# Optimization experiments

Measured on AMD Instinct MI355X. Metric: run time of the kernel, lower is better.

## Reference

```python
import jax, jax.numpy as jnp
import numpy as np
import math

NUM_EXPERTS = 8
CAP_FACTOR = 1.25
MIN_CAPACITY = 4

def _capacity(num_tokens, num_experts):
    cap = math.floor(CAP_FACTOR * num_tokens / num_experts)
    cap += cap % 2
    return max(cap, MIN_CAPACITY)

def setup_inputs() -> dict:
    key = jax.random.key(0)
    k1, k2, k3, k4 = jax.random.split(key, 4)
    tokens, d_model, d_ff, E = 8192, 1024, 4096, NUM_EXPERTS
    x = jax.random.normal(k1, (tokens, d_model), dtype=jnp.float32)
    gate_weight = jax.random.normal(k2, (E, d_model), dtype=jnp.float32) * math.sqrt(0.1 / d_model)
    expert_weight = jax.random.normal(k3, (E, d_model, d_ff), dtype=jnp.float32) * 0.02
    expert_bias = jax.random.normal(k4, (E, 1, d_ff), dtype=jnp.float32) * 0.02
    return {"x": x, "gate_weight": gate_weight, "expert_weight": expert_weight, "expert_bias": expert_bias}

def reference(x, gate_weight, expert_weight, expert_bias):
    tokens, d_model = x.shape
    E = gate_weight.shape[0]
    capacity = _capacity(tokens, E)
    # FP32 gate (Switch-style)
    gate_logits = jnp.dot(x.astype(jnp.float32), gate_weight.astype(jnp.float32).T)  # [s, E]
    logits = jax.nn.softmax(gate_logits, axis=-1)  # auto_cast_softmax in fp32
    # Top-1 routing, select_policy='first'
    top1_idx = jnp.argmax(gate_logits, axis=-1)  # argmax over raw gate output
    mask = jax.nn.one_hot(top1_idx, E, dtype=jnp.int32)  # [s, E]
    # aux load-balancing loss (training path)
    me = jnp.mean(logits, axis=0)
    ce = jnp.mean(mask.astype(jnp.float32), axis=0)
    l_aux = E * jnp.sum(me * ce)
    # cumsum-based capacity ranking
    ranks = jnp.cumsum(mask, axis=0) - 1  # [s, E]
    mask = mask * (ranks < capacity).astype(jnp.int32)
    ranks_tok = jnp.sum(mask * ranks, axis=-1)  # [s]
    rank_oh = jax.nn.one_hot(ranks_tok, capacity, dtype=logits.dtype)  # [s, c]
    weight = mask.astype(logits.dtype) * logits  # [s, E]
    combine_weights = weight[:, :, None] * rank_oh[:, None, :]  # [s, E, c]
    sec_mask = combine_weights != 0  # bool dispatch mask
    # scatter dispatch: [s,E,c] x [s,d] -> [E,c,d]
    dispatched = jnp.einsum("sec,sd->ecd", sec_mask.astype(x.dtype), x)
    # per-expert front linear: [E,c,d] x [E,d,f] -> [E,c,f]
    out = jnp.einsum("ecd,edf->ecf", dispatched, expert_weight) + expert_bias
    return out, combine_weights, l_aux
```

## Files before the change

### kernel.cpp

```cpp
#include <hip/hip_runtime.h>
#include <hip/hip_bf16.h>

#define TOKENS 8192
#define DM 1024
#define DFF 4096
#define NE 8
#define CAP 1280
#define ECAP (NE*CAP)
#define OUT_ELEMS ((size_t)NE*CAP*DFF)
#define CMB_ELEMS ((size_t)TOKENS*NE*CAP)
#define ZROW TOKENS
#define GBK 32

typedef __attribute__((ext_vector_type(8))) short short8;
typedef __attribute__((ext_vector_type(16))) float f32x16;
typedef __attribute__((ext_vector_type(4))) float f4;

__device__ inline ushort f2bf(float f) {
    __hip_bfloat16 h = __float2bfloat16(f);
    return *reinterpret_cast<ushort*>(&h);
}

__device__ __forceinline__ void gload16(const ushort* g, short* l) {
    __builtin_amdgcn_global_load_lds(
        (const __attribute__((address_space(1))) void*)g,
        (__attribute__((address_space(3))) void*)l, 16, 0, 0);
}

__global__ __launch_bounds__(256) void gate_kernel(const float* __restrict__ x,
        const float* __restrict__ gw, float* __restrict__ probs8, int* __restrict__ top1,
        ushort* __restrict__ xbf) {
    int wave = threadIdx.x >> 6;
    int lane = threadIdx.x & 63;
    int t = blockIdx.x * 4 + wave;
    const float* xrow = x + (size_t)t * DM;
    float4 xv[4];
    #pragma unroll
    for (int j = 0; j < 4; ++j) xv[j] = *(const float4*)(xrow + lane * 4 + j * 256);
    ushort* xbrow = xbf + (size_t)t * DM;
    #pragma unroll
    for (int j = 0; j < 4; ++j) {
        ushort4 o;
        o.x = f2bf(xv[j].x); o.y = f2bf(xv[j].y); o.z = f2bf(xv[j].z); o.w = f2bf(xv[j].w);
        *(ushort4*)(xbrow + lane * 4 + j * 256) = o;
    }
    float logit[8];
    #pragma unroll
    for (int e = 0; e < 8; ++e) {
        const float* g = gw + e * DM;
        float s = 0.f;
        #pragma unroll
        for (int j = 0; j < 4; ++j) {
            float4 gv = *(const float4*)(g + lane * 4 + j * 256);
            s += xv[j].x * gv.x + xv[j].y * gv.y + xv[j].z * gv.z + xv[j].w * gv.w;
        }
        #pragma unroll
        for (int off = 32; off >= 1; off >>= 1) s += __shfl_xor(s, off);
        logit[e] = s;
    }
    if (lane == 0) {
        int bi = 0; float bv = logit[0];
        #pragma unroll
        for (int e = 1; e < 8; ++e) if (logit[e] > bv) { bv = logit[e]; bi = e; }
        float se = 0.f, p[8];
        #pragma unroll
        for (int e = 0; e < 8; ++e) { p[e] = expf(logit[e] - bv); se += p[e]; }
        float inv = 1.f / se;
        #pragma unroll
        for (int e = 0; e < 8; ++e) probs8[t * 8 + e] = p[e] * inv;
        top1[t] = bi;
    }
    if (blockIdx.x == 0) {
        ushort4 z; z.x = z.y = z.z = z.w = 0;
        *(ushort4*)(xbf + (size_t)ZROW * DM + threadIdx.x * 4) = z;
    }
}

__global__ __launch_bounds__(512) void cvtw_rank_kernel(
        const float* __restrict__ w, ushort* __restrict__ wt,
        const int* __restrict__ top1, const float* __restrict__ probs8,
        int* __restrict__ slot_token, int* __restrict__ pos,
        int* __restrict__ cnts, float* __restrict__ laux_out) {
    __shared__ __align__(16) char smem[TOKENS * 4 + 64 * 4 + 8 * 4];
    const int tid = threadIdx.x;
    if (blockIdx.x == 0) {
        int* t1s = (int*)smem;
        float* red = (float*)(smem + TOKENS * 4);
        int* cnt_sh = (int*)(smem + TOKENS * 4 + 64 * 4);
        int w8 = tid >> 6;
        int lane = tid & 63;
        for (int i = tid; i < TOKENS; i += 512) t1s[i] = top1[i];
        for (int i = tid; i < ECAP; i += 512) slot_token[i] = ZROW;
        for (int i = tid; i < TOKENS; i += 512) pos[i] = -1;

        float ps[8];
        #pragma unroll
        for (int e = 0; e < 8; ++e) ps[e] = 0.f;
        for (int t = tid; t < TOKENS; t += 512) {
            float4 a = *(const float4*)(probs8 + t * 8);
            float4 b = *(const float4*)(probs8 + t * 8 + 4);
            ps[0] += a.x; ps[1] += a.y; ps[2] += a.z; ps[3] += a.w;
            ps[4] += b.x; ps[5] += b.y; ps[6] += b.z; ps[7] += b.w;
        }
        #pragma unroll
        for (int e = 0; e < 8; ++e) {
            #pragma unroll
            for (int off = 32; off >= 1; off >>= 1) ps[e] += __shfl_xor(ps[e], off);
        }
        if (lane == 0) {
            #pragma unroll
            for (int e = 0; e < 8; ++e) red[w8 * 8 + e] = ps[e];
        }
        __syncthreads();

        int base = 0;
        for (int t0 = 0; t0 < TOKENS; t0 += 256) {
            #pragma unroll
            for (int q = 0; q < 4; ++q) {
                int t = t0 + q * 64 + lane;
                bool mine = (t1s[t] == w8);
                unsigned long long m = __ballot(mine);
                if (mine) {
                    int r = base + __popcll(m & ((1ull << lane) - 1ull));
                    if (r < CAP) { slot_token[w8 * CAP + r] = t; pos[t] = w8 * CAP + r; }
                }
                base += __popcll(m);
            }
        }
        if (lane == 0) { cnt_sh[w8] = base; cnts[w8] = (base < CAP) ? base : CAP; }
        __syncthreads();
        if (tid == 0) {
            float la = 0.f;
            #pragma unroll
            for (int e = 0; e < 8; ++e) {
                float me = 0.f;
                #pragma unroll
                for (int wv = 0; wv < 8; ++wv) me += red[wv * 8 + e];
                la += (me / (float)TOKENS) * ((float)cnt_sh[e] / (float)TOKENS);
            }
            laux_out[0] = la * (float)NE;
        }
        return;
    }
    float (*tile)[65] = (float(*)[65])smem;
    int b = blockIdx.x - 1;
    int e = b >> 11;
    int rem = b & 2047;
    int n0 = (rem & 63) * 64;
    int k0 = (rem >> 6) * 32;
    const float* we = w + (size_t)e * DM * DFF;
    int c = tid & 63, r0 = tid >> 6;
    #pragma unroll
    for (int i = 0; i < 4; ++i) {
        int r = r0 + i * 8;
        tile[r][c] = we[(size_t)(k0 + r) * DFF + n0 + c];
    }
    __syncthreads();
    ushort* wte = wt + (size_t)e * DFF * DM;
    int kc = tid & 31, nr0 = tid >> 5;
    #pragma unroll
    for (int i = 0; i < 4; ++i) {
        int nr = nr0 + i * 16;
        wte[(size_t)(n0 + nr) * DM + k0 + kc] = f2bf(tile[kc][nr]);
    }
}

__global__ __launch_bounds__(512, 2) void gemm_kernel(
    const ushort* __restrict__ xbf,
    const ushort* __restrict__ wt,
    const float*  __restrict__ bias,
    const int*    __restrict__ slot_token,
    const int*    __restrict__ cnts,
    float* __restrict__ out,
    const int*    __restrict__ pos,
    const float*  __restrict__ probs8,
    float* __restrict__ cmb,
    int do_combine)
{
    const int bid = blockIdx.x;
    const int e   = bid & 7;
    const int rem = bid >> 3;
    const int nt  = rem & 15;
    const int mt  = rem >> 4;
    __shared__ __align__(16) short lds[4][16384];
    const int tid  = threadIdx.x;
    const int lane = tid & 63;
    const int wave = tid >> 6;
    const int wr = wave >> 2;
    const int wc = wave & 3;
    const int ln31 = lane & 31, lh = lane >> 5;
    const int tbeg = bid * 16;
    const bool has_cmb = do_combine && (bid < 512);

    float* orow = out + ((size_t)(e * CAP + mt * 256)) * DFF + (size_t)nt * 256;

    if (mt * 256 >= cnts[e]) {
        int c4 = tid & 63;
        int r0b = tid >> 6;
        f4 bv4 = *(const f4*)(bias + e * DFF + nt * 256 + c4 * 4);
        for (int r = r0b; r < 256; r += 8)
            __builtin_nontemporal_store(bv4, (f4*)(orow + (size_t)r * DFF + c4 * 4));
        if (has_cmb) {
            for (int i = 0; i < 16; ++i) {
                int tok = tbeg + i;
                int p = pos[tok];
                int ee = (p < 0) ? 0 : (p / CAP);
                float val = probs8[tok * 8 + ee];
                f4* row = (f4*)(cmb + (size_t)tok * ECAP);
                #pragma unroll
                for (int k = 0; k < 5; ++k) {
                    int b4 = (tid + k * 512) * 4;
                    f4 v;
                    v.x = (b4 + 0 == p) ? val : 0.f;
                    v.y = (b4 + 1 == p) ? val : 0.f;
                    v.z = (b4 + 2 == p) ? val : 0.f;
                    v.w = (b4 + 3 == p) ? val : 0.f;
                    __builtin_nontemporal_store(v, row + tid + k * 512);
                }
            }
        }
        return;
    }

    const int r0 = tid >> 2;
    const int kg = (tid & 3) ^ ((tid >> 3) & 3);
    const int tokA0 = slot_token[e * CAP + mt * 256 + r0];
    const int tokA1 = slot_token[e * CAP + mt * 256 + 128 + r0];
    const ushort* aptr0 = xbf + (size_t)tokA0 * DM + kg * 8;
    const ushort* aptr1 = xbf + (size_t)tokA1 * DM + kg * 8;
    const ushort* bptr0 = wt + ((size_t)e * DFF + (size_t)nt * 256 + r0) * DM + kg * 8;
    const ushort* bptr1 = bptr0 + (size_t)128 * DM;

    #define STAGE(T) do { \
        short* base_ = &lds[(T) & 3][0]; \
        size_t ko_ = (size_t)(T) * GBK; \
        gload16(aptr0 + ko_, base_ + tid * 8); \
        gload16(aptr1 + ko_, base_ + 4096 + tid * 8); \
        gload16(bptr0 + ko_, base_ + 8192 + tid * 8); \
        gload16(bptr1 + ko_, base_ + 12288 + tid * 8); \
    } while (0)

    int aoff[8], boff[4];
    #pragma unroll
    for (int s = 0; s < 2; ++s) {
        #pragma unroll
        for (int mi = 0; mi < 4; ++mi) {
            int r = wr * 128 + mi * 32 + ln31;
            int c = lh + 2 * s;
            aoff[s * 4 + mi] = (r * 4 + (c ^ ((r >> 1) & 3))) * 8;
        }
        #pragma unroll
        for (int ni = 0; ni < 2; ++ni) {
            int rn = wc * 64 + ni * 32 + ln31;
            int c = lh + 2 * s;
            boff[s * 2 + ni] = 8192 + (rn * 4 + (c ^ ((rn >> 1) & 3))) * 8;
        }
    }

    f4* cmb_p = (f4*)cmb + (size_t)tbeg * (ECAP / 4);
    int kpart = 0, ntok = 0;
    int cur_p = -1, nxt_p = -1;
    float cur_val = 0.f, nxt_val = 0.f;
    if (has_cmb) {
        cur_p = pos[tbeg];
        { int ee = (cur_p < 0) ? 0 : (cur_p / CAP); cur_val = probs8[tbeg * 8 + ee]; }
        nxt_p = pos[tbeg + 1];
        { int ee = (nxt_p < 0) ? 0 : (nxt_p / CAP); nxt_val = probs8[(tbeg + 1) * 8 + ee]; }
    }
    #define CSTORE() do { if (has_cmb) { \
        int b4_ = (tid + kpart * 512) * 4; \
        f4 v_; \
        v_.x = (b4_ + 0 == cur_p) ? cur_val : 0.f; \
        v_.y = (b4_ + 1 == cur_p) ? cur_val : 0.f; \
        v_.z = (b4_ + 2 == cur_p) ? cur_val : 0.f; \
        v_.w = (b4_ + 3 == cur_p) ? cur_val : 0.f; \
        __builtin_nontemporal_store(v_, cmb_p + tid + kpart * 512); \
        if (++kpart == 5) { \
            kpart = 0; cmb_p += ECAP / 4; ++ntok; \
            cur_p = nxt_p; cur_val = nxt_val; \
            if (ntok + 1 < 16) { \
                nxt_p = pos[tbeg + ntok + 1]; \
                int ee_ = (nxt_p < 0) ? 0 : (nxt_p / CAP); \
                nxt_val = probs8[(tbeg + ntok + 1) * 8 + ee_]; \
            } \
        } \
    } } while (0)

    f32x16 acc[4][2];
    #pragma unroll
    for (int mi = 0; mi < 4; ++mi)
        #pragma unroll
        for (int ni = 0; ni < 2; ++ni)
            acc[mi][ni] = (f32x16)(0.f);

    STAGE(0); STAGE(1); STAGE(2);
    for (int t = 0; t < 32; ++t) {
        if (t < 29) {
            STAGE(t + 3);
            asm volatile("s_waitcnt vmcnt(12)" ::: "memory");
        } else if (t == 29) {
            asm volatile("s_waitcnt vmcnt(8)" ::: "memory");
        } else if (t == 30) {
            asm volatile("s_waitcnt vmcnt(4)" ::: "memory");
        } else {
            asm volatile("s_waitcnt vmcnt(0)" ::: "memory");
        }
        __builtin_amdgcn_s_barrier();
        __builtin_amdgcn_sched_barrier(0);

        const short* L = &lds[t & 3][0];
        __builtin_amdgcn_s_setprio(1);
        #pragma unroll
        for (int s = 0; s < 2; ++s) {
            short8 af[4], bfr[2];
            #pragma unroll
            for (int ni = 0; ni < 2; ++ni) bfr[ni] = *(const short8*)(L + boff[s * 2 + ni]);
            #pragma unroll
            for (int mi = 0; mi < 4; ++mi) af[mi] = *(const short8*)(L + aoff[s * 4 + mi]);
            #pragma unroll
            for (int mi = 0; mi < 4; ++mi)
                #pragma unroll
                for (int ni = 0; ni < 2; ++ni)
                    acc[mi][ni] = __builtin_amdgcn_mfma_f32_32x32x16_bf16(af[mi], bfr[ni], acc[mi][ni], 0, 0, 0);
        }
        __builtin_amdgcn_s_setprio(0);
        CSTORE(); CSTORE();
        if (t < 16) CSTORE();
        __builtin_amdgcn_sched_barrier(0);
        asm volatile("" ::: "memory");
        __builtin_amdgcn_s_barrier();
        asm volatile("" ::: "memory");
    }
    #undef STAGE
    #undef CSTORE

    #pragma unroll
    for (int ni = 0; ni < 2; ++ni) {
        int c = wc * 64 + ni * 32 + ln31;
        float bv = bias[e * DFF + nt * 256 + c];
        #pragma unroll
        for (int mi = 0; mi < 4; ++mi) {
            #pragma unroll
            for (int reg = 0; reg < 16; ++reg) {
                int r = wr * 128 + mi * 32 + (reg & 3) + 8 * (reg >> 2) + 4 * lh;
                __builtin_nontemporal_store(acc[mi][ni][reg] + bv,
                    orow + (size_t)r * DFF + c);
            }
        }
    }
}

__global__ __launch_bounds__(256) void combine_kernel(const int* __restrict__ pos,
        const float* __restrict__ probs8, float* __restrict__ cmb) {
    int tok = blockIdx.x;
    int p = pos[tok];
    int e = p / CAP;
    float val = probs8[tok * 8 + (e < 0 ? 0 : e)];
    f4* row = (f4*)(cmb + (size_t)tok * ECAP);
    #pragma unroll
    for (int k = 0; k < 10; ++k) {
        int c = threadIdx.x + k * 256;
        int b4 = c * 4;
        f4 v;
        v.x = (b4 + 0 == p) ? val : 0.f;
        v.y = (b4 + 1 == p) ? val : 0.f;
        v.z = (b4 + 2 == p) ? val : 0.f;
        v.w = (b4 + 3 == p) ? val : 0.f;
        __builtin_nontemporal_store(v, row + c);
    }
}

extern "C" void kernel_launch(void* const* d_in, const int* in_sizes, int n_in,
                              void* d_out, int out_size, void* d_ws, size_t ws_size,
                              hipStream_t stream) {
    const float* x  = (const float*)d_in[0];
    const float* gw = (const float*)d_in[1];
    const float* ew = (const float*)d_in[2];
    const float* eb = (const float*)d_in[3];

    float* out = (float*)d_out;
    float* cmb = out + OUT_ELEMS;
    float* laux_out = cmb + CMB_ELEMS;

    float* probs8 = (float*)d_ws;
    int* top1 = (int*)(probs8 + TOKENS * 8);
    int* slot_token = top1 + TOKENS;
    int* pos = slot_token + ECAP;
    int* cnts = pos + TOKENS;

    const size_t SMALL = 1 << 20;
    const size_t WT_ELEMS_ = (size_t)NE * DFF * DM;
    const size_t XBF_ELEMS_ = (size_t)(TOKENS + 1) * DM;
    bool big_ws = ws_size >= SMALL + (WT_ELEMS_ + XBF_ELEMS_) * sizeof(ushort);
    ushort* wtbf = big_ws ? (ushort*)((char*)d_ws + SMALL) : (ushort*)cmb;
    ushort* xbf  = wtbf + WT_ELEMS_;

    gate_kernel<<<TOKENS / 4, 256, 0, stream>>>(x, gw, probs8, top1, xbf);
    cvtw_rank_kernel<<<16385, 512, 0, stream>>>(ew, wtbf, top1, probs8,
                                                slot_token, pos, cnts, laux_out);
    if (big_ws) {
        gemm_kernel<<<640, 512, 0, stream>>>(xbf, wtbf, eb, slot_token, cnts, out,
                                             pos, probs8, cmb, 1);
    } else {
        gemm_kernel<<<640, 512, 0, stream>>>(xbf, wtbf, eb, slot_token, cnts, out,
                                             pos, probs8, cmb, 0);
        combine_kernel<<<TOKENS, 256, 0, stream>>>(pos, probs8, cmb);
    }
}
```

Measured before the change: 193.2 us.

## Shrink GEMM tiles to 128x128 with 256 threads and double buffering

The expert GEMM tile drops from 256x256 with 512 threads and a 4-stage LDS pipeline to 128x128 with 256 threads and a 2-stage pipeline, spread over 2560 blocks. Each block writes its combine-weight rows after the GEMM instead of interleaving the stores inside the k-loop. The aim is more blocks per CU and better load balance across the ragged per-expert token counts. In exchange, each tile reuses its operands less, issues more global loads per flop, and has a shallower prefetch depth to hide latency.

```diff
diff --git a/kernel.cpp b/kernel.cpp
--- a/kernel.cpp
+++ b/kernel.cpp
@@ -165,7 +165,7 @@
     }
 }
 
-__global__ __launch_bounds__(512, 2) void gemm_kernel(
+__global__ __launch_bounds__(256, 3) void gemm_kernel(
     const ushort* __restrict__ xbf,
     const ushort* __restrict__ wt,
     const float*  __restrict__ bias,
@@ -180,171 +180,135 @@
     const int bid = blockIdx.x;
     const int e   = bid & 7;
     const int rem = bid >> 3;
-    const int nt  = rem & 15;
-    const int mt  = rem >> 4;
-    __shared__ __align__(16) short lds[4][16384];
+    const int nt  = rem & 31;
+    const int mt  = rem >> 5;
+    __shared__ __align__(16) short lds[2][8192];
     const int tid  = threadIdx.x;
     const int lane = tid & 63;
     const int wave = tid >> 6;
-    const int wr = wave >> 2;
-    const int wc = wave & 3;
+    const int wr = wave >> 1;
+    const int wc = wave & 1;
     const int ln31 = lane & 31, lh = lane >> 5;
-    const int tbeg = bid * 16;
-    const bool has_cmb = do_combine && (bid < 512);
-
-    float* orow = out + ((size_t)(e * CAP + mt * 256)) * DFF + (size_t)nt * 256;
-
-    if (mt * 256 >= cnts[e]) {
-        int c4 = tid & 63;
-        int r0b = tid >> 6;
-        f4 bv4 = *(const f4*)(bias + e * DFF + nt * 256 + c4 * 4);
-        for (int r = r0b; r < 256; r += 8)
+    const int tbeg = bid * 4;
+    const bool has_cmb = do_combine && (bid < 2048);
+
+    float* orow = out + ((size_t)(e * CAP + mt * 128)) * DFF + (size_t)nt * 128;
+
+    if (mt * 128 >= cnts[e]) {
+        int c4 = tid & 31;
+        int r0b = tid >> 5;
+        f4 bv4 = *(const f4*)(bias + e * DFF + nt * 128 + c4 * 4);
+        for (int r = r0b; r < 128; r += 8)
             __builtin_nontemporal_store(bv4, (f4*)(orow + (size_t)r * DFF + c4 * 4));
-        if (has_cmb) {
-            for (int i = 0; i < 16; ++i) {
-                int tok = tbeg + i;
-                int p = pos[tok];
-                int ee = (p < 0) ? 0 : (p / CAP);
-                float val = probs8[tok * 8 + ee];
-                f4* row = (f4*)(cmb + (size_t)tok * ECAP);
-                #pragma unroll
-                for (int k = 0; k < 5; ++k) {
-                    int b4 = (tid + k * 512) * 4;
-                    f4 v;
-                    v.x = (b4 + 0 == p) ? val : 0.f;
-                    v.y = (b4 + 1 == p) ? val : 0.f;
-                    v.z = (b4 + 2 == p) ? val : 0.f;
-                    v.w = (b4 + 3 == p) ? val : 0.f;
-                    __builtin_nontemporal_store(v, row + tid + k * 512);
+    } else {
+        const int r0 = tid >> 2;
+        const int kg = (tid & 3) ^ ((tid >> 3) & 3);
+        const int tokA0 = slot_token[e * CAP + mt * 128 + r0];
+        const int tokA1 = slot_token[e * CAP + mt * 128 + 64 + r0];
+        const ushort* aptr0 = xbf + (size_t)tokA0 * DM + kg * 8;
+        const ushort* aptr1 = xbf + (size_t)tokA1 * DM + kg * 8;
+        const ushort* bptr0 = wt + ((size_t)e * DFF + (size_t)nt * 128 + r0) * DM + kg * 8;
+        const ushort* bptr1 = bptr0 + (size_t)64 * DM;
+
+        #define STAGE(T) do { \
+            short* base_ = &lds[(T) & 1][0]; \
+            size_t ko_ = (size_t)(T) * GBK; \
+            gload16(aptr0 + ko_, base_ + tid * 8); \
+            gload16(aptr1 + ko_, base_ + 2048 + tid * 8); \
+            gload16(bptr0 + ko_, base_ + 4096 + tid * 8); \
+            gload16(bptr1 + ko_, base_ + 6144 + tid * 8); \
+        } while (0)
+
+        int aoff[4], boff[4];
+        #pragma unroll
+        for (int s = 0; s < 2; ++s) {
+            #pragma unroll
+            for (int mi = 0; mi < 2; ++mi) {
+                int r = wr * 64 + mi * 32 + ln31;
+                int c = lh + 2 * s;
+                aoff[s * 2 + mi] = (r * 4 + (c ^ ((r >> 1) & 3))) * 8;
+            }
+            #pragma unroll
+            for (int ni = 0; ni < 2; ++ni) {
+                int rn = wc * 64 + ni * 32 + ln31;
+                int c = lh + 2 * s;
+                boff[s * 2 + ni] = 4096 + (rn * 4 + (c ^ ((rn >> 1) & 3))) * 8;
+            }
+        }
+
+        f32x16 acc[2][2];
+        #pragma unroll
+        for (int mi = 0; mi < 2; ++mi)
+            #pragma unroll
+            for (int ni = 0; ni < 2; ++ni)
+                acc[mi][ni] = (f32x16)(0.f);
+
+        STAGE(0);
+        for (int t = 0; t < 32; ++t) {
+            if (t < 31) {
+                STAGE(t + 1);
+                asm volatile("s_waitcnt vmcnt(4)" ::: "memory");
+            } else {
+                asm volatile("s_waitcnt vmcnt(0)" ::: "memory");
+            }
+            __builtin_amdgcn_s_barrier();
+            __builtin_amdgcn_sched_barrier(0);
+
+            const short* L = &lds[t & 1][0];
+            __builtin_amdgcn_s_setprio(1);
+            #pragma unroll
+            for (int s = 0; s < 2; ++s) {
+                short8 af[2], bfr[2];
+                #pragma unroll
+                for (int ni = 0; ni < 2; ++ni) bfr[ni] = *(const short8*)(L + boff[s * 2 + ni]);
+                #pragma unroll
+                for (int mi = 0; mi < 2; ++mi) af[mi] = *(const short8*)(L + aoff[s * 2 + mi]);
+                #pragma unroll
+                for (int mi = 0; mi < 2; ++mi)
+                    #pragma unroll
+                    for (int ni = 0; ni < 2; ++ni)
+                        acc[mi][ni] = __builtin_amdgcn_mfma_f32_32x32x16_bf16(af[mi], bfr[ni], acc[mi][ni], 0, 0, 0);
+            }
+            __builtin_amdgcn_s_setprio(0);
+            __builtin_amdgcn_sched_barrier(0);
+            asm volatile("" ::: "memory");
+            __builtin_amdgcn_s_barrier();
+            asm volatile("" ::: "memory");
+        }
+        #undef STAGE
+
+        #pragma unroll
+        for (int ni = 0; ni < 2; ++ni) {
+            int c = wc * 64 + ni * 32 + ln31;
+            float bv = bias[e * DFF + nt * 128 + c];
+            #pragma unroll
+            for (int mi = 0; mi < 2; ++mi) {
+                #pragma unroll
+                for (int reg = 0; reg < 16; ++reg) {
+                    int r = wr * 64 + mi * 32 + (reg & 3) + 8 * (reg >> 2) + 4 * lh;
+                    __builtin_nontemporal_store(acc[mi][ni][reg] + bv,
+                        orow + (size_t)r * DFF + c);
                 }
             }
         }
-        return;
-    }
-
-    const int r0 = tid >> 2;
-    const int kg = (tid & 3) ^ ((tid >> 3) & 3);
-    const int tokA0 = slot_token[e * CAP + mt * 256 + r0];
-    const int tokA1 = slot_token[e * CAP + mt * 256 + 128 + r0];
-    const ushort* aptr0 = xbf + (size_t)tokA0 * DM + kg * 8;
-    const ushort* aptr1 = xbf + (size_t)tokA1 * DM + kg * 8;
-    const ushort* bptr0 = wt + ((size_t)e * DFF + (size_t)nt * 256 + r0) * DM + kg * 8;
-    const ushort* bptr1 = bptr0 + (size_t)128 * DM;
-
-    #define STAGE(T) do { \
-        short* base_ = &lds[(T) & 3][0]; \
-        size_t ko_ = (size_t)(T) * GBK; \
-        gload16(aptr0 + ko_, base_ + tid * 8); \
-        gload16(aptr1 + ko_, base_ + 4096 + tid * 8); \
-        gload16(bptr0 + ko_, base_ + 8192 + tid * 8); \
-        gload16(bptr1 + ko_, base_ + 12288 + tid * 8); \
-    } while (0)
-
-    int aoff[8], boff[4];
-    #pragma unroll
-    for (int s = 0; s < 2; ++s) {
-        #pragma unroll
-        for (int mi = 0; mi < 4; ++mi) {
-            int r = wr * 128 + mi * 32 + ln31;
-            int c = lh + 2 * s;
-            aoff[s * 4 + mi] = (r * 4 + (c ^ ((r >> 1) & 3))) * 8;
-        }
-        #pragma unroll
-        for (int ni = 0; ni < 2; ++ni) {
-            int rn = wc * 64 + ni * 32 + ln31;
-            int c = lh + 2 * s;
-            boff[s * 2 + ni] = 8192 + (rn * 4 + (c ^ ((rn >> 1) & 3))) * 8;
-        }
-    }
-
-    f4* cmb_p = (f4*)cmb + (size_t)tbeg * (ECAP / 4);
-    int kpart = 0, ntok = 0;
-    int cur_p = -1, nxt_p = -1;
-    float cur_val = 0.f, nxt_val = 0.f;
+    }
+
     if (has_cmb) {
-        cur_p = pos[tbeg];
-        { int ee = (cur_p < 0) ? 0 : (cur_p / CAP); cur_val = probs8[tbeg * 8 + ee]; }
-        nxt_p = pos[tbeg + 1];
-        { int ee = (nxt_p < 0) ? 0 : (nxt_p / CAP); nxt_val = probs8[(tbeg + 1) * 8 + ee]; }
-    }
-    #define CSTORE() do { if (has_cmb) { \
-        int b4_ = (tid + kpart * 512) * 4; \
-        f4 v_; \
-        v_.x = (b4_ + 0 == cur_p) ? cur_val : 0.f; \
-        v_.y = (b4_ + 1 == cur_p) ? cur_val : 0.f; \
-        v_.z = (b4_ + 2 == cur_p) ? cur_val : 0.f; \
-        v_.w = (b4_ + 3 == cur_p) ? cur_val : 0.f; \
-        __builtin_nontemporal_store(v_, cmb_p + tid + kpart * 512); \
-        if (++kpart == 5) { \
-            kpart = 0; cmb_p += ECAP / 4; ++ntok; \
-            cur_p = nxt_p; cur_val = nxt_val; \
-            if (ntok + 1 < 16) { \
-                nxt_p = pos[tbeg + ntok + 1]; \
-                int ee_ = (nxt_p < 0) ? 0 : (nxt_p / CAP); \
-                nxt_val = probs8[(tbeg + ntok + 1) * 8 + ee_]; \
-            } \
-        } \
-    } } while (0)
-
-    f32x16 acc[4][2];
-    #pragma unroll
-    for (int mi = 0; mi < 4; ++mi)
-        #pragma unroll
-        for (int ni = 0; ni < 2; ++ni)
-            acc[mi][ni] = (f32x16)(0.f);
-
-    STAGE(0); STAGE(1); STAGE(2);
-    for (int t = 0; t < 32; ++t) {
-        if (t < 29) {
-            STAGE(t + 3);
-            asm volatile("s_waitcnt vmcnt(12)" ::: "memory");
-        } else if (t == 29) {
-            asm volatile("s_waitcnt vmcnt(8)" ::: "memory");
-        } else if (t == 30) {
-            asm volatile("s_waitcnt vmcnt(4)" ::: "memory");
-        } else {
-            asm volatile("s_waitcnt vmcnt(0)" ::: "memory");
-        }
-        __builtin_amdgcn_s_barrier();
-        __builtin_amdgcn_sched_barrier(0);
-
-        const short* L = &lds[t & 3][0];
-        __builtin_amdgcn_s_setprio(1);
-        #pragma unroll
-        for (int s = 0; s < 2; ++s) {
-            short8 af[4], bfr[2];
-            #pragma unroll
-            for (int ni = 0; ni < 2; ++ni) bfr[ni] = *(const short8*)(L + boff[s * 2 + ni]);
-            #pragma unroll
-            for (int mi = 0; mi < 4; ++mi) af[mi] = *(const short8*)(L + aoff[s * 4 + mi]);
-            #pragma unroll
-            for (int mi = 0; mi < 4; ++mi)
-                #pragma unroll
-                for (int ni = 0; ni < 2; ++ni)
-                    acc[mi][ni] = __builtin_amdgcn_mfma_f32_32x32x16_bf16(af[mi], bfr[ni], acc[mi][ni], 0, 0, 0);
-        }
-        __builtin_amdgcn_s_setprio(0);
-        CSTORE(); CSTORE();
-        if (t < 16) CSTORE();
-        __builtin_amdgcn_sched_barrier(0);
-        asm volatile("" ::: "memory");
-        __builtin_amdgcn_s_barrier();
-        asm volatile("" ::: "memory");
-    }
-    #undef STAGE
-    #undef CSTORE
-
-    #pragma unroll
-    for (int ni = 0; ni < 2; ++ni) {
-        int c = wc * 64 + ni * 32 + ln31;
-        float bv = bias[e * DFF + nt * 256 + c];
-        #pragma unroll
-        for (int mi = 0; mi < 4; ++mi) {
-            #pragma unroll
-            for (int reg = 0; reg < 16; ++reg) {
-                int r = wr * 128 + mi * 32 + (reg & 3) + 8 * (reg >> 2) + 4 * lh;
-                __builtin_nontemporal_store(acc[mi][ni][reg] + bv,
-                    orow + (size_t)r * DFF + c);
+        for (int i = 0; i < 4; ++i) {
+            int tok = tbeg + i;
+            int p = pos[tok];
+            int ee = (p < 0) ? 0 : (p / CAP);
+            float val = probs8[tok * 8 + ee];
+            f4* row = (f4*)(cmb + (size_t)tok * ECAP);
+            #pragma unroll
+            for (int k = 0; k < 10; ++k) {
+                int b4 = (tid + k * 256) * 4;
+                f4 v;
+                v.x = (b4 + 0 == p) ? val : 0.f;
+                v.y = (b4 + 1 == p) ? val : 0.f;
+                v.z = (b4 + 2 == p) ? val : 0.f;
+                v.w = (b4 + 3 == p) ? val : 0.f;
+                __builtin_nontemporal_store(v, row + tid + k * 256);
             }
         }
     }
@@ -399,11 +363,11 @@
     cvtw_rank_kernel<<<16385, 512, 0, stream>>>(ew, wtbf, top1, probs8,
                                                 slot_token, pos, cnts, laux_out);
     if (big_ws) {
-        gemm_kernel<<<640, 512, 0, stream>>>(xbf, wtbf, eb, slot_token, cnts, out,
-                                             pos, probs8, cmb, 1);
+        gemm_kernel<<<2560, 256, 0, stream>>>(xbf, wtbf, eb, slot_token, cnts, out,
+                                              pos, probs8, cmb, 1);
     } else {
-        gemm_kernel<<<640, 512, 0, stream>>>(xbf, wtbf, eb, slot_token, cnts, out,
-                                             pos, probs8, cmb, 0);
+        gemm_kernel<<<2560, 256, 0, stream>>>(xbf, wtbf, eb, slot_token, cnts, out,
+                                              pos, probs8, cmb, 0);
         combine_kernel<<<TOKENS, 256, 0, stream>>>(pos, probs8, cmb);
     }
 }
```

Result: slower. 202.7 us (+4.9%).
